# Kernel optimization log

Hardware: AMD Instinct MI355X
Metric: run time of the kernel (lower is better)

Reference implementation:

```python
import jax, jax.numpy as jnp
import numpy as np

N_NODES = 100000
N_EDGES = 1600000
IN_FEATURES = 256
OUT_FEATURES = 64


def setup_inputs() -> dict:
    key = jax.random.key(0)
    k_x, k_r, k_c, k_v, k_w = jax.random.split(key, 5)
    x = jax.random.normal(k_x, (N_NODES, IN_FEATURES), dtype=jnp.float32)
    adj_rows = jax.random.randint(k_r, (N_EDGES,), 0, N_NODES, dtype=jnp.int64)
    adj_cols = jax.random.randint(k_c, (N_EDGES,), 0, N_NODES, dtype=jnp.int64)
    adj_vals = jax.random.uniform(k_v, (N_EDGES,), dtype=jnp.float32)
    # Glorot-uniform init as in reset_parameters()
    init_range = np.sqrt(6.0 / (IN_FEATURES + OUT_FEATURES)).astype(np.float32)
    W = jax.random.uniform(k_w, (IN_FEATURES, OUT_FEATURES), dtype=jnp.float32,
                           minval=-init_range, maxval=init_range)
    return {"x": x, "adj_rows": adj_rows, "adj_cols": adj_cols,
            "adj_vals": adj_vals, "W": W}


def reference(x, adj_rows, adj_cols, adj_vals, W):
    # support = x @ W  : dense [N, in] x [in, out]
    support = x @ W  # [N, out]
    # output = adj @ support : COO SpMM via gather + segment-sum
    # msgs[e] = adj_vals[e] * support[col[e]]
    msgs = adj_vals[:, None] * support[adj_cols]  # [E, out]
    output = jax.ops.segment_sum(msgs, adj_rows, num_segments=N_NODES)  # [N, out]
    return output
```

## Files before the change

### kernel.cpp

```cpp
#include <hip/hip_runtime.h>


#define KDIM 256
#define MDIM 64
#define BSHIFT 7
#define BMAX 1024
#define FCAP 6500

__global__ __launch_bounds__(256) void gemm_xw(
    const float* __restrict__ x, const float* __restrict__ W,
    float* __restrict__ support, int nrows)
{
    __shared__ float xs[128][64];
    __shared__ float ws2[64][64];
    const int tid = threadIdx.x;
    const int tr  = tid >> 4;
    const int f0  = (tid & 15) * 4;
    const int swz = tr & 3;
    const int row0 = blockIdx.x * 128;

    float acc[8][4];
    #pragma unroll
    for (int i = 0; i < 8; ++i)
        #pragma unroll
        for (int j = 0; j < 4; ++j) acc[i][j] = 0.f;

    for (int kt = 0; kt < KDIM; kt += 64) {
        __syncthreads();
        #pragma unroll
        for (int i = 0; i < 8; ++i) {
            int slot = tid + i * 256;
            int r = slot >> 4;
            int q = slot & 15;
            int grow = row0 + r;
            float4 v = make_float4(0.f, 0.f, 0.f, 0.f);
            if (grow < nrows)
                v = *reinterpret_cast<const float4*>(
                        &x[(size_t)grow * KDIM + kt + q * 4]);
            int qs = q ^ ((r >> 3) & 3);
            *reinterpret_cast<float4*>(&xs[r][qs * 4]) = v;
        }
        #pragma unroll
        for (int i = 0; i < 4; ++i) {
            int slot = tid + i * 256;
            int kk = slot >> 4;
            int q = slot & 15;
            float4 v = *reinterpret_cast<const float4*>(
                           &W[(size_t)(kt + kk) * MDIM + q * 4]);
            *reinterpret_cast<float4*>(&ws2[kk][q * 4]) = v;
        }
        __syncthreads();

        #pragma unroll 2
        for (int kk = 0; kk < 64; kk += 4) {
            const int q4 = kk >> 2;
            float4 xv[8];
            #pragma unroll
            for (int i = 0; i < 8; ++i)
                xv[i] = *reinterpret_cast<const float4*>(
                            &xs[tr * 8 + i][(q4 ^ swz) * 4]);
            #pragma unroll
            for (int k2 = 0; k2 < 4; ++k2) {
                float4 wv = *reinterpret_cast<const float4*>(&ws2[kk + k2][f0]);
                #pragma unroll
                for (int i = 0; i < 8; ++i) {
                    const float xk = (k2 == 0) ? xv[i].x :
                                     (k2 == 1) ? xv[i].y :
                                     (k2 == 2) ? xv[i].z : xv[i].w;
                    acc[i][0] = fmaf(xk, wv.x, acc[i][0]);
                    acc[i][1] = fmaf(xk, wv.y, acc[i][1]);
                    acc[i][2] = fmaf(xk, wv.z, acc[i][2]);
                    acc[i][3] = fmaf(xk, wv.w, acc[i][3]);
                }
            }
        }
    }

    #pragma unroll
    for (int i = 0; i < 8; ++i) {
        int grow = row0 + tr * 8 + i;
        if (grow < nrows) {
            float4 v = make_float4(acc[i][0], acc[i][1], acc[i][2], acc[i][3]);
            *reinterpret_cast<float4*>(&support[(size_t)grow * MDIM + f0]) = v;
        }
    }
}

__global__ __launch_bounds__(256) void coarse_hist(
    const int* __restrict__ rows, int* __restrict__ counts,
    int nedges, int nbuckets)
{
    __shared__ int lb[BMAX];
    const int t = threadIdx.x;
    for (int i = t; i < nbuckets; i += 256) lb[i] = 0;
    __syncthreads();
    int e = blockIdx.x * 256 + t;
    const int stride = gridDim.x * 256;
    for (; e < nedges; e += stride)
        atomicAdd(&lb[rows[e] >> BSHIFT], 1);
    __syncthreads();
    for (int i = t; i < nbuckets; i += 256) {
        int c = lb[i];
        if (c) atomicAdd(&counts[i], c);
    }
}

__global__ __launch_bounds__(256) void coarse_scan(
    const int* __restrict__ counts, int* __restrict__ offsets,
    int* __restrict__ cursor, int n)
{
    __shared__ int sh[256];
    const int t = threadIdx.x;
    const int base = t * 4;
    int v0 = 0, v1 = 0, v2 = 0, v3 = 0;
    if (base + 0 < n) v0 = counts[base + 0];
    if (base + 1 < n) v1 = counts[base + 1];
    if (base + 2 < n) v2 = counts[base + 2];
    if (base + 3 < n) v3 = counts[base + 3];
    const int tsum = v0 + v1 + v2 + v3;
    sh[t] = tsum;
    __syncthreads();
    for (int off = 1; off < 256; off <<= 1) {
        int xv = (t >= off) ? sh[t - off] : 0;
        __syncthreads();
        sh[t] += xv;
        __syncthreads();
    }
    int excl = sh[t] - tsum;
    if (base + 0 < n) { offsets[base + 0] = excl; cursor[base + 0] = excl; } excl += v0;
    if (base + 1 < n) { offsets[base + 1] = excl; cursor[base + 1] = excl; } excl += v1;
    if (base + 2 < n) { offsets[base + 2] = excl; cursor[base + 2] = excl; } excl += v2;
    if (base + 3 < n) { offsets[base + 3] = excl; cursor[base + 3] = excl; }
}

__global__ __launch_bounds__(256) void bin_edges(
    const int* __restrict__ rows, const int* __restrict__ cols,
    const float* __restrict__ vals, int* __restrict__ cursor,
    int2* __restrict__ edata, int nedges, int nbuckets)
{
    __shared__ int lb[BMAX];
    const int t = threadIdx.x;
    const int per = (nedges + gridDim.x - 1) / gridDim.x;
    const int e0 = blockIdx.x * per;
    const int e1 = min(e0 + per, nedges);

    for (int i = t; i < nbuckets; i += 256) lb[i] = 0;
    __syncthreads();
    for (int e = e0 + t; e < e1; e += 256)
        atomicAdd(&lb[rows[e] >> BSHIFT], 1);
    __syncthreads();
    for (int i = t; i < nbuckets; i += 256) {
        int c = lb[i];
        lb[i] = c ? atomicAdd(&cursor[i], c) : 0;
    }
    __syncthreads();
    for (int e = e0 + t; e < e1; e += 256) {
        const int r = rows[e];
        const int pos = atomicAdd(&lb[r >> BSHIFT], 1);
        int2 pk;
        pk.x = (cols[e] & 0x1FFFF) | ((r & 127) << 17);
        pk.y = __float_as_int(vals[e]);
        edata[pos] = pk;
    }
}

__global__ __launch_bounds__(256) void fine_scatter(
    const int* __restrict__ offsets, const int* __restrict__ counts,
    int2* __restrict__ edata, int* __restrict__ foff, int* __restrict__ fcnt,
    int* __restrict__ bflag, int nrows)
{
    __shared__ int2 lrec[FCAP];
    __shared__ int cnt[128];
    __shared__ int cur[128];
    __shared__ int sh[128];
    const int t = threadIdx.x;
    const int b = blockIdx.x;
    const int beg = offsets[b];
    const int cntE = counts[b];
    const int row0 = b << BSHIFT;

    if (t < 128) cnt[t] = 0;
    __syncthreads();

    if (cntE > FCAP) {
        if (t == 0) bflag[b] = 1;
        if (t < 128) {
            const int grow = row0 + t;
            if (grow < nrows) { foff[grow] = beg; fcnt[grow] = 0; }
        }
        return;
    }

    for (int k = t; k < cntE; k += 256) {
        int2 p = edata[beg + k];
        lrec[k] = p;
        atomicAdd(&cnt[(p.x >> 17) & 127], 1);
    }
    __syncthreads();

    if (t < 128) sh[t] = cnt[t];
    __syncthreads();
    for (int off = 1; off < 128; off <<= 1) {
        int xv = 0;
        if (t < 128 && t >= off) xv = sh[t - off];
        __syncthreads();
        if (t < 128) sh[t] += xv;
        __syncthreads();
    }
    if (t < 128) {
        const int excl = sh[t] - cnt[t];
        cur[t] = excl;
        const int grow = row0 + t;
        if (grow < nrows) { foff[grow] = beg + excl; fcnt[grow] = cnt[t]; }
    }
    __syncthreads();

    for (int k = t; k < cntE; k += 256) {
        const int2 p = lrec[k];
        const int rl = (p.x >> 17) & 127;
        const int pos = beg + atomicAdd(&cur[rl], 1);
        edata[pos] = make_int2(p.x & 0x1FFFF, p.y);
    }
}

__global__ __launch_bounds__(256) void spmm_reduce(
    const int* __restrict__ foff, const int* __restrict__ fcnt,
    const int2* __restrict__ edata, const float* __restrict__ support,
    float* __restrict__ out, int nrows)
{
    const int g = blockIdx.x * 16 + (threadIdx.x >> 4);
    const int f0 = (threadIdx.x & 15) * 4;
    if (g >= nrows) return;
    int e = foff[g];
    const int end = e + fcnt[g];
    float ax = 0.f, ay = 0.f, az = 0.f, aw = 0.f;

    for (; e + 4 <= end; e += 4) {
        const int2 p0 = edata[e + 0];
        const int2 p1 = edata[e + 1];
        const int2 p2 = edata[e + 2];
        const int2 p3 = edata[e + 3];
        float4 s0 = *reinterpret_cast<const float4*>(
                        &support[(size_t)p0.x * MDIM + f0]);
        float4 s1 = *reinterpret_cast<const float4*>(
                        &support[(size_t)p1.x * MDIM + f0]);
        float4 s2 = *reinterpret_cast<const float4*>(
                        &support[(size_t)p2.x * MDIM + f0]);
        float4 s3 = *reinterpret_cast<const float4*>(
                        &support[(size_t)p3.x * MDIM + f0]);
        const float v0 = __int_as_float(p0.y);
        const float v1 = __int_as_float(p1.y);
        const float v2 = __int_as_float(p2.y);
        const float v3 = __int_as_float(p3.y);
        ax = fmaf(v0, s0.x, ax); ay = fmaf(v0, s0.y, ay);
        az = fmaf(v0, s0.z, az); aw = fmaf(v0, s0.w, aw);
        ax = fmaf(v1, s1.x, ax); ay = fmaf(v1, s1.y, ay);
        az = fmaf(v1, s1.z, az); aw = fmaf(v1, s1.w, aw);
        ax = fmaf(v2, s2.x, ax); ay = fmaf(v2, s2.y, ay);
        az = fmaf(v2, s2.z, az); aw = fmaf(v2, s2.w, aw);
        ax = fmaf(v3, s3.x, ax); ay = fmaf(v3, s3.y, ay);
        az = fmaf(v3, s3.z, az); aw = fmaf(v3, s3.w, aw);
    }
    for (; e < end; ++e) {
        const int2 p = edata[e];
        const float v = __int_as_float(p.y);
        float4 s = *reinterpret_cast<const float4*>(
                       &support[(size_t)p.x * MDIM + f0]);
        ax = fmaf(v, s.x, ax); ay = fmaf(v, s.y, ay);
        az = fmaf(v, s.z, az); aw = fmaf(v, s.w, aw);
    }
    *reinterpret_cast<float4*>(&out[(size_t)g * MDIM + f0]) =
        make_float4(ax, ay, az, aw);
}

__global__ __launch_bounds__(256) void scatter_tail(
    const int* __restrict__ offsets, const int* __restrict__ counts,
    const int* __restrict__ bflag, const int2* __restrict__ edata,
    const float* __restrict__ support, float* __restrict__ out)
{
    const int b = blockIdx.x;
    if (!bflag[b]) return;
    const int beg = offsets[b];
    const int end = beg + counts[b];
    const int row0 = b << BSHIFT;
    const int g  = threadIdx.x >> 4;
    const int f0 = (threadIdx.x & 15) * 4;
    for (int e = beg + g; e < end; e += 16) {
        const int2 p = edata[e];
        const int c = p.x & 0x1FFFF;
        const int r = row0 + ((p.x >> 17) & 127);
        const float v = __int_as_float(p.y);
        float4 s = *reinterpret_cast<const float4*>(
                       &support[(size_t)c * MDIM + f0]);
        float* op = &out[(size_t)r * MDIM + f0];
        atomicAdd(op + 0, v * s.x);
        atomicAdd(op + 1, v * s.y);
        atomicAdd(op + 2, v * s.z);
        atomicAdd(op + 3, v * s.w);
    }
}

__global__ __launch_bounds__(256) void scatter_edges(
    const int* __restrict__ rows, const int* __restrict__ cols,
    const float* __restrict__ vals, const float* __restrict__ support,
    float* __restrict__ out, int nedges)
{
    const int t = blockIdx.x * blockDim.x + threadIdx.x;
    const int fq = (t & 15) * 4;
    int e = t >> 4;
    const int estride = (gridDim.x * blockDim.x) >> 4;
    for (; e < nedges; e += estride) {
        const int r = rows[e];
        const int c = cols[e];
        const float v = vals[e];
        float4 s = *reinterpret_cast<const float4*>(
                       &support[(size_t)c * MDIM + fq]);
        float* op = &out[(size_t)r * MDIM + fq];
        atomicAdd(op + 0, v * s.x);
        atomicAdd(op + 1, v * s.y);
        atomicAdd(op + 2, v * s.z);
        atomicAdd(op + 3, v * s.w);
    }
}

extern "C" void kernel_launch(void* const* d_in, const int* in_sizes, int n_in,
                              void* d_out, int out_size, void* d_ws, size_t ws_size,
                              hipStream_t stream) {
    const float* x    = (const float*)d_in[0];
    const int*   rows = (const int*)d_in[1];
    const int*   cols = (const int*)d_in[2];
    const float* vals = (const float*)d_in[3];
    const float* W    = (const float*)d_in[4];
    float* out = (float*)d_out;

    const int nnodes = in_sizes[0] / KDIM;
    const int nedges = in_sizes[1];
    const int nbuckets = (nnodes + 127) >> BSHIFT;

    auto align256 = [](size_t v) { return (v + 255) & ~(size_t)255; };
    const size_t sz_support = align256((size_t)nnodes * MDIM * 4);
    const size_t sz_bkt     = align256((size_t)BMAX * 4);
    const size_t sz_nodes   = align256((size_t)nnodes * 4);
    const size_t sz_edata   = align256((size_t)nedges * 8);
    const size_t need = sz_support + 4 * sz_bkt + 2 * sz_nodes + sz_edata;

    char* w = (char*)d_ws;
    float* support = (float*)w;  w += sz_support;

    gemm_xw<<<dim3((nnodes + 127) / 128), dim3(256), 0, stream>>>(
        x, W, support, nnodes);

    if (ws_size >= need && nbuckets <= BMAX && nnodes <= (1 << 17)) {
        int* counts  = (int*)w;  w += sz_bkt;
        int* offsets = (int*)w;  w += sz_bkt;
        int* cursor  = (int*)w;  w += sz_bkt;
        int* bflag   = (int*)w;  w += sz_bkt;
        int* foff    = (int*)w;  w += sz_nodes;
        int* fcnt    = (int*)w;  w += sz_nodes;
        int2* edata  = (int2*)w;

        hipMemsetAsync(counts, 0, (size_t)nbuckets * 4, stream);
        hipMemsetAsync(bflag, 0, (size_t)nbuckets * 4, stream);

        coarse_hist<<<dim3(256), dim3(256), 0, stream>>>(
            rows, counts, nedges, nbuckets);
        coarse_scan<<<dim3(1), dim3(256), 0, stream>>>(
            counts, offsets, cursor, nbuckets);
        bin_edges<<<dim3(256), dim3(256), 0, stream>>>(
            rows, cols, vals, cursor, edata, nedges, nbuckets);
        fine_scatter<<<dim3(nbuckets), dim3(256), 0, stream>>>(
            offsets, counts, edata, foff, fcnt, bflag, nnodes);
        spmm_reduce<<<dim3((nnodes + 15) / 16), dim3(256), 0, stream>>>(
            foff, fcnt, edata, support, out, nnodes);
        scatter_tail<<<dim3(nbuckets), dim3(256), 0, stream>>>(
            offsets, counts, bflag, edata, support, out);
    } else {
        hipMemsetAsync(d_out, 0, (size_t)out_size * sizeof(float), stream);
        scatter_edges<<<dim3(4096), dim3(256), 0, stream>>>(
            rows, cols, vals, support, out, nedges);
    }
}
```

Before: 367.2 us.

## Double-buffer GEMM with direct global-to-LDS loads and deepen SpMM gather unroll

The x@W kernel now loads tiles straight from global memory into LDS with global_load_lds, double-buffers 16-wide K slices so loads overlap compute, and grows each block to 256 rows with an 8x8 register tile per thread. This targets load latency and the register round-trip of staging through VGPRs, and raises FMA work per LDS read. The SpMM reduce loop gathers 8 edges per iteration instead of 4 to keep more memory requests in flight. The cost is higher register pressure and fewer blocks in the GEMM grid.

```diff
diff --git a/kernel.cpp b/kernel.cpp
--- a/kernel.cpp
+++ b/kernel.cpp
@@ -7,81 +7,106 @@
 #define BMAX 1024
 #define FCAP 6500
 
-__global__ __launch_bounds__(256) void gemm_xw(
+__device__ __forceinline__ void gld_lds16(const float* g, float* l) {
+    __builtin_amdgcn_global_load_lds(
+        (const __attribute__((address_space(1))) unsigned int*)g,
+        (__attribute__((address_space(3))) unsigned int*)l, 16, 0, 0);
+}
+
+__global__ __launch_bounds__(256, 3) void gemm_xw(
     const float* __restrict__ x, const float* __restrict__ W,
     float* __restrict__ support, int nrows)
 {
-    __shared__ float xs[128][64];
-    __shared__ float ws2[64][64];
-    const int tid = threadIdx.x;
-    const int tr  = tid >> 4;
-    const int f0  = (tid & 15) * 4;
-    const int swz = tr & 3;
-    const int row0 = blockIdx.x * 128;
-
-    float acc[8][4];
+    __shared__ float lds[2][5120];
+    const int tid  = threadIdx.x;
+    const int lane = tid & 63;
+    const int wid  = tid >> 6;
+    const int rg   = tid >> 3;
+    const int fg   = tid & 7;
+    const int r0   = rg * 8;
+    const int f0   = fg * 8;
+    const int sk   = rg & 3;
+    const int row0 = blockIdx.x * 256;
+
+    float acc[8][8];
     #pragma unroll
     for (int i = 0; i < 8; ++i)
         #pragma unroll
-        for (int j = 0; j < 4; ++j) acc[i][j] = 0.f;
-
-    for (int kt = 0; kt < KDIM; kt += 64) {
-        __syncthreads();
-        #pragma unroll
-        for (int i = 0; i < 8; ++i) {
-            int slot = tid + i * 256;
-            int r = slot >> 4;
-            int q = slot & 15;
-            int grow = row0 + r;
-            float4 v = make_float4(0.f, 0.f, 0.f, 0.f);
-            if (grow < nrows)
-                v = *reinterpret_cast<const float4*>(
-                        &x[(size_t)grow * KDIM + kt + q * 4]);
-            int qs = q ^ ((r >> 3) & 3);
-            *reinterpret_cast<float4*>(&xs[r][qs * 4]) = v;
-        }
-        #pragma unroll
-        for (int i = 0; i < 4; ++i) {
-            int slot = tid + i * 256;
-            int kk = slot >> 4;
-            int q = slot & 15;
-            float4 v = *reinterpret_cast<const float4*>(
-                           &W[(size_t)(kt + kk) * MDIM + q * 4]);
-            *reinterpret_cast<float4*>(&ws2[kk][q * 4]) = v;
-        }
-        __syncthreads();
-
-        #pragma unroll 2
-        for (int kk = 0; kk < 64; kk += 4) {
-            const int q4 = kk >> 2;
+        for (int j = 0; j < 8; ++j) acc[i][j] = 0.f;
+
+    auto stage = [&](int bf, int kt) {
+        #pragma unroll
+        for (int j = 0; j < 4; ++j) {
+            const int ig  = wid * 4 + j;
+            const int row = ig * 16 + (lane >> 2);
+            const int kq  = (lane & 3) ^ ((row >> 3) & 3);
+            const int gr  = min(row0 + row, nrows - 1);
+            gld_lds16(x + (size_t)gr * KDIM + kt + kq * 4,
+                      &lds[bf][ig * 256]);
+        }
+        {
+            const int kk = wid * 4 + (lane >> 4);
+            const int fq = lane & 15;
+            gld_lds16(W + (size_t)(kt + kk) * MDIM + fq * 4,
+                      &lds[bf][4096 + wid * 256]);
+        }
+    };
+
+    auto compute = [&](int bf) {
+        const float* xs = &lds[bf][0];
+        const float* ws = &lds[bf][4096];
+        #pragma unroll
+        for (int q = 0; q < 4; ++q) {
             float4 xv[8];
+            const int slot = q ^ sk;
             #pragma unroll
             for (int i = 0; i < 8; ++i)
                 xv[i] = *reinterpret_cast<const float4*>(
-                            &xs[tr * 8 + i][(q4 ^ swz) * 4]);
+                            &xs[(r0 + i) * 16 + slot * 4]);
             #pragma unroll
             for (int k2 = 0; k2 < 4; ++k2) {
-                float4 wv = *reinterpret_cast<const float4*>(&ws2[kk + k2][f0]);
+                const int kk = q * 4 + k2;
+                const float4 wa = *reinterpret_cast<const float4*>(
+                                      &ws[kk * 64 + f0]);
+                const float4 wb = *reinterpret_cast<const float4*>(
+                                      &ws[kk * 64 + f0 + 4]);
                 #pragma unroll
                 for (int i = 0; i < 8; ++i) {
                     const float xk = (k2 == 0) ? xv[i].x :
                                      (k2 == 1) ? xv[i].y :
                                      (k2 == 2) ? xv[i].z : xv[i].w;
-                    acc[i][0] = fmaf(xk, wv.x, acc[i][0]);
-                    acc[i][1] = fmaf(xk, wv.y, acc[i][1]);
-                    acc[i][2] = fmaf(xk, wv.z, acc[i][2]);
-                    acc[i][3] = fmaf(xk, wv.w, acc[i][3]);
+                    acc[i][0] = fmaf(xk, wa.x, acc[i][0]);
+                    acc[i][1] = fmaf(xk, wa.y, acc[i][1]);
+                    acc[i][2] = fmaf(xk, wa.z, acc[i][2]);
+                    acc[i][3] = fmaf(xk, wa.w, acc[i][3]);
+                    acc[i][4] = fmaf(xk, wb.x, acc[i][4]);
+                    acc[i][5] = fmaf(xk, wb.y, acc[i][5]);
+                    acc[i][6] = fmaf(xk, wb.z, acc[i][6]);
+                    acc[i][7] = fmaf(xk, wb.w, acc[i][7]);
                 }
             }
         }
+    };
+
+    stage(0, 0);
+    __syncthreads();
+    int bf = 0;
+    #pragma unroll 1
+    for (int t = 0; t < KDIM / 16; ++t) {
+        if (t < KDIM / 16 - 1) stage(bf ^ 1, (t + 1) * 16);
+        compute(bf);
+        __syncthreads();
+        bf ^= 1;
     }
 
     #pragma unroll
     for (int i = 0; i < 8; ++i) {
-        int grow = row0 + tr * 8 + i;
+        const int grow = row0 + r0 + i;
         if (grow < nrows) {
-            float4 v = make_float4(acc[i][0], acc[i][1], acc[i][2], acc[i][3]);
-            *reinterpret_cast<float4*>(&support[(size_t)grow * MDIM + f0]) = v;
+            *reinterpret_cast<float4*>(&support[(size_t)grow * MDIM + f0]) =
+                make_float4(acc[i][0], acc[i][1], acc[i][2], acc[i][3]);
+            *reinterpret_cast<float4*>(&support[(size_t)grow * MDIM + f0 + 4]) =
+                make_float4(acc[i][4], acc[i][5], acc[i][6], acc[i][7]);
         }
     }
 }
@@ -235,31 +260,21 @@
     const int end = e + fcnt[g];
     float ax = 0.f, ay = 0.f, az = 0.f, aw = 0.f;
 
-    for (; e + 4 <= end; e += 4) {
-        const int2 p0 = edata[e + 0];
-        const int2 p1 = edata[e + 1];
-        const int2 p2 = edata[e + 2];
-        const int2 p3 = edata[e + 3];
-        float4 s0 = *reinterpret_cast<const float4*>(
-                        &support[(size_t)p0.x * MDIM + f0]);
-        float4 s1 = *reinterpret_cast<const float4*>(
-                        &support[(size_t)p1.x * MDIM + f0]);
-        float4 s2 = *reinterpret_cast<const float4*>(
-                        &support[(size_t)p2.x * MDIM + f0]);
-        float4 s3 = *reinterpret_cast<const float4*>(
-                        &support[(size_t)p3.x * MDIM + f0]);
-        const float v0 = __int_as_float(p0.y);
-        const float v1 = __int_as_float(p1.y);
-        const float v2 = __int_as_float(p2.y);
-        const float v3 = __int_as_float(p3.y);
-        ax = fmaf(v0, s0.x, ax); ay = fmaf(v0, s0.y, ay);
-        az = fmaf(v0, s0.z, az); aw = fmaf(v0, s0.w, aw);
-        ax = fmaf(v1, s1.x, ax); ay = fmaf(v1, s1.y, ay);
-        az = fmaf(v1, s1.z, az); aw = fmaf(v1, s1.w, aw);
-        ax = fmaf(v2, s2.x, ax); ay = fmaf(v2, s2.y, ay);
-        az = fmaf(v2, s2.z, az); aw = fmaf(v2, s2.w, aw);
-        ax = fmaf(v3, s3.x, ax); ay = fmaf(v3, s3.y, ay);
-        az = fmaf(v3, s3.z, az); aw = fmaf(v3, s3.w, aw);
+    for (; e + 8 <= end; e += 8) {
+        int2 p[8];
+        #pragma unroll
+        for (int u = 0; u < 8; ++u) p[u] = edata[e + u];
+        float4 s[8];
+        #pragma unroll
+        for (int u = 0; u < 8; ++u)
+            s[u] = *reinterpret_cast<const float4*>(
+                       &support[(size_t)p[u].x * MDIM + f0]);
+        #pragma unroll
+        for (int u = 0; u < 8; ++u) {
+            const float v = __int_as_float(p[u].y);
+            ax = fmaf(v, s[u].x, ax); ay = fmaf(v, s[u].y, ay);
+            az = fmaf(v, s[u].z, az); aw = fmaf(v, s[u].w, aw);
+        }
     }
     for (; e < end; ++e) {
         const int2 p = edata[e];
@@ -347,7 +362,7 @@
     char* w = (char*)d_ws;
     float* support = (float*)w;  w += sz_support;
 
-    gemm_xw<<<dim3((nnodes + 127) / 128), dim3(256), 0, stream>>>(
+    gemm_xw<<<dim3((nnodes + 255) / 256), dim3(256), 0, stream>>>(
         x, W, support, nnodes);
 
     if (ws_size >= need && nbuckets <= BMAX && nnodes <= (1 << 17)) {
```

Result: slower. 391.5 us (+6.6%).
